# Optimization experiments

Hardware: AMD Instinct MI355X
Metric: run time of the kernel (lower is better)

Reference implementation:

```python
import jax, jax.numpy as jnp
import numpy as np

B, NPTS, T, P, C, D = 2, 32768, 32768, 512, 4, 768


def _sincos_pos_embed(centers, embed_dim):
    # centers: np [P,3]; matches get_3d_sincos_pos_embed
    c = centers - centers.mean(axis=0)
    c = c / np.linalg.norm(c, axis=1).max()
    div = np.exp(np.arange(0, embed_dim, 6) * -(np.log(10000.0) / embed_dim))  # [D/6]
    arg = c[:, None, :] * div[None, :, None]                                   # [P, D/6, 3]
    pe = np.concatenate([np.sin(arg), np.cos(arg)], axis=-1).reshape(centers.shape[0], embed_dim)
    return pe.astype(np.float32)


def setup_inputs() -> dict:
    key = jax.random.key(0)
    ks = jax.random.split(key, 12)
    rng = np.random.default_rng(0)

    # ragged patch sizes (avg 64) summing exactly to T
    sizes = rng.integers(32, 97, size=P).astype(np.int64)
    sizes = np.maximum((sizes * (T / sizes.sum())).astype(np.int64), 1)
    sizes[-1] += T - sizes.sum()
    patch_offset = jnp.asarray(np.concatenate([[0], np.cumsum(sizes)]), dtype=jnp.int32)  # [P+1]

    patch_index = jax.random.randint(ks[0], (T,), 0, NPTS, dtype=jnp.int32)
    latent = jax.random.normal(ks[1], (B, NPTS, C), dtype=jnp.float32)

    s = 0.02
    params = dict(
        w1a=jax.random.normal(ks[2], (C, D), jnp.float32) * s,
        b1a=jnp.zeros((D,), jnp.float32),
        w1b=jax.random.normal(ks[3], (D, D), jnp.float32) * s,
        b1b=jnp.zeros((D,), jnp.float32),
        w2a=jax.random.normal(ks[4], (2 * D, D), jnp.float32) * s,
        b2a=jnp.zeros((D,), jnp.float32),
        g2=jnp.ones((D,), jnp.float32),
        beta2=jnp.zeros((D,), jnp.float32),
        w2b=jax.random.normal(ks[5], (D, D), jnp.float32) * s,
        b2b=jnp.zeros((D,), jnp.float32),
    )

    centers = rng.standard_normal((P, 3))
    pos_embed = jnp.asarray(_sincos_pos_embed(centers, D))[None]  # [1, P, D]

    return dict(latent=latent, patch_index=patch_index, patch_offset=patch_offset,
                pos_embed=pos_embed, **params)


def _ln(x, eps, gamma=None, beta=None):
    mu = x.mean(axis=-1, keepdims=True)
    var = ((x - mu) ** 2).mean(axis=-1, keepdims=True)
    y = (x - mu) * jax.lax.rsqrt(var + eps)
    if gamma is not None:
        y = y * gamma + beta
    return y


def reference(latent, patch_index, patch_offset, pos_embed,
              w1a, b1a, w1b, b1b, w2a, b2a, g2, beta2, w2b, b2b):
    T_ = patch_index.shape[0]
    P_ = patch_offset.shape[0] - 1
    # segment id of each token (repeat_interleave inverse): seg[t] = patch containing t
    seg = jnp.searchsorted(patch_offset[1:], jnp.arange(T_, dtype=patch_offset.dtype), side='right')

    x = latent[:, patch_index, :]                           # [B, T, C] gather
    h = x @ w1a + b1a
    h = jax.nn.gelu(_ln(h, 1e-6), approximate=False)
    h = h @ w1b + b1b                                       # [B, T, D]

    segmax = lambda a: jax.ops.segment_max(a, seg, num_segments=P_)
    y = jax.vmap(segmax)(h)                                 # [B, P, D] ragged max-pool

    h2 = jnp.concatenate([y[:, seg, :], h], axis=-1)        # repeat_interleave + concat
    h2 = h2 @ w2a + b2a
    h2 = jax.nn.gelu(_ln(h2, 1e-5, g2, beta2), approximate=False)
    h2 = h2 @ w2b + b2b                                     # [B, T, D]
    raw_latent = h2

    out = jax.vmap(segmax)(raw_latent) + pos_embed          # [B, P, D]
    return out.astype(raw_latent.dtype), raw_latent
```

## Files before the change

### kernel.cpp

```cpp
#include <hip/hip_runtime.h>
#include <hip/hip_bf16.h>
#include <math.h>

#define B_    2
#define NPTS_ 32768
#define T_    32768
#define P_    512
#define C_    4
#define D_    768
#define M_    (B_ * T_)

typedef __bf16 bf16_t;
typedef __bf16 bf16x8 __attribute__((ext_vector_type(8)));
typedef __bf16 bf16x4 __attribute__((ext_vector_type(4)));
typedef float  f32x4  __attribute__((ext_vector_type(4)));

__device__ inline void gload16(const void* g, void* l) {
  __builtin_amdgcn_global_load_lds(
      (const __attribute__((address_space(1))) void*)g,
      (__attribute__((address_space(3))) void*)l, 16, 0, 0);
}

__device__ inline float gelu_exact(float x) {
  return 0.5f * x * (1.0f + erff(x * 0.70710678118654752f));
}

__device__ inline unsigned fmap(float x) {
  unsigned u = __float_as_uint(x);
  return (u & 0x80000000u) ? ~u : (u | 0x80000000u);
}
__device__ inline float funmap(unsigned u) {
  unsigned v = (u & 0x80000000u) ? (u & 0x7FFFFFFFu) : ~u;
  return __uint_as_float(v);
}

__global__ void seg_kernel(const int* __restrict__ off, int* __restrict__ seg) {
  int t = blockIdx.x * blockDim.x + threadIdx.x;
  if (t >= T_) return;
  int lo = 0, hi = P_;
  while (lo < hi) {
    int mid = (lo + hi) >> 1;
    if (off[mid + 1] <= t) lo = mid + 1; else hi = mid;
  }
  seg[t] = lo;
}

__global__ __launch_bounds__(256) void init_umax_kernel(uint4* __restrict__ u) {
  u[blockIdx.x * 256 + threadIdx.x] = make_uint4(0, 0, 0, 0);
}

__global__ __launch_bounds__(256) void yconv_kernel(
    const uint4* __restrict__ ymax, bf16_t* __restrict__ y) {
  int t = blockIdx.x * 256 + threadIdx.x;
  uint4 u = ymax[t];
  bf16x4 o;
  o[0] = (bf16_t)funmap(u.x); o[1] = (bf16_t)funmap(u.y);
  o[2] = (bf16_t)funmap(u.z); o[3] = (bf16_t)funmap(u.w);
  *(bf16x4*)(y + (size_t)t * 4) = o;
}

__global__ __launch_bounds__(256) void final2_kernel(
    const uint4* __restrict__ rmax, const float4* __restrict__ pe,
    float4* __restrict__ out) {
  int t = blockIdx.x * 256 + threadIdx.x;
  int row = t / 192, col = t % 192;
  uint4 u = rmax[t];
  float4 p = pe[(row & (P_ - 1)) * 192 + col];
  float4 o;
  o.x = funmap(u.x) + p.x; o.y = funmap(u.y) + p.y;
  o.z = funmap(u.z) + p.z; o.w = funmap(u.w) + p.w;
  out[t] = o;
}

__global__ __launch_bounds__(256) void wconvT_kernel(
    const float* __restrict__ src, bf16_t* __restrict__ dst, int K, int N) {
  __shared__ float tile[32][33];
  int n0 = blockIdx.x * 32, k0 = blockIdx.y * 32;
  int tx = threadIdx.x, ty = threadIdx.y;
  #pragma unroll
  for (int i = 0; i < 4; ++i)
    tile[ty + 8 * i][tx] = src[(size_t)(k0 + ty + 8 * i) * N + n0 + tx];
  __syncthreads();
  #pragma unroll
  for (int i = 0; i < 4; ++i)
    dst[(size_t)(n0 + ty + 8 * i) * K + k0 + tx] = (bf16_t)tile[tx][ty + 8 * i];
}

__global__ __launch_bounds__(256) void embed_kernel(
    const float4* __restrict__ latent4, const int* __restrict__ pidx,
    const float* __restrict__ w1a, const float* __restrict__ b1a,
    bf16_t* __restrict__ act1) {
  int wid = threadIdx.x >> 6, lane = threadIdx.x & 63;
  int m = blockIdx.x * 4 + wid;
  int b = m >> 15, t = m & (T_ - 1);
  float4 x = latent4[(size_t)b * NPTS_ + pidx[t]];
  int d8 = lane * 8, d4 = 512 + lane * 4;
  float v[12];
  {
    float4 a0 = *(const float4*)(b1a + d8);
    float4 a1 = *(const float4*)(b1a + d8 + 4);
    float4 a2 = *(const float4*)(b1a + d4);
    v[0]=a0.x; v[1]=a0.y; v[2]=a0.z; v[3]=a0.w;
    v[4]=a1.x; v[5]=a1.y; v[6]=a1.z; v[7]=a1.w;
    v[8]=a2.x; v[9]=a2.y; v[10]=a2.z; v[11]=a2.w;
  }
  float xk[4] = {x.x, x.y, x.z, x.w};
  #pragma unroll
  for (int k = 0; k < 4; ++k) {
    const float* w = w1a + k * D_;
    float4 w0 = *(const float4*)(w + d8);
    float4 w1 = *(const float4*)(w + d8 + 4);
    float4 w2 = *(const float4*)(w + d4);
    float f = xk[k];
    v[0] += f*w0.x; v[1] += f*w0.y; v[2] += f*w0.z; v[3] += f*w0.w;
    v[4] += f*w1.x; v[5] += f*w1.y; v[6] += f*w1.z; v[7] += f*w1.w;
    v[8] += f*w2.x; v[9] += f*w2.y; v[10]+= f*w2.z; v[11]+= f*w2.w;
  }
  float sum = 0.f, sq = 0.f;
  #pragma unroll
  for (int j = 0; j < 12; ++j) { sum += v[j]; sq += v[j]*v[j]; }
  #pragma unroll
  for (int o = 32; o > 0; o >>= 1) { sum += __shfl_xor(sum, o); sq += __shfl_xor(sq, o); }
  float mu = sum * (1.0f / D_);
  float rstd = rsqrtf(sq * (1.0f / D_) - mu * mu + 1e-6f);
  bf16x8 o8; bf16x4 o4;
  #pragma unroll
  for (int j = 0; j < 8; ++j) o8[j] = (bf16_t)gelu_exact((v[j] - mu) * rstd);
  #pragma unroll
  for (int j = 0; j < 4; ++j) o4[j] = (bf16_t)gelu_exact((v[8 + j] - mu) * rstd);
  size_t base = (size_t)m * D_;
  *(bf16x8*)(act1 + base + d8) = o8;
  *(bf16x4*)(act1 + base + d4) = o4;
}

__global__ __launch_bounds__(256) void ln2_kernel(
    const bf16_t* __restrict__ h2pre, const float* __restrict__ z,
    const int* __restrict__ seg, const float* __restrict__ g2,
    const float* __restrict__ beta2, bf16_t* __restrict__ act2) {
  int wid = threadIdx.x >> 6, lane = threadIdx.x & 63;
  int m = blockIdx.x * 4 + wid;
  int b = m >> 15, t = m & (T_ - 1);
  int d8 = lane * 8, d4 = 512 + lane * 4;
  size_t base = (size_t)m * D_;
  const float* zrow = z + (size_t)((b << 9) + seg[t]) * D_;
  bf16x8 i8 = *(const bf16x8*)(h2pre + base + d8);
  bf16x4 i4 = *(const bf16x4*)(h2pre + base + d4);
  float4 z0 = *(const float4*)(zrow + d8);
  float4 z1 = *(const float4*)(zrow + d8 + 4);
  float4 z2 = *(const float4*)(zrow + d4);
  float v[12];
  #pragma unroll
  for (int j = 0; j < 8; ++j) v[j] = (float)i8[j];
  #pragma unroll
  for (int j = 0; j < 4; ++j) v[8 + j] = (float)i4[j];
  v[0]+=z0.x; v[1]+=z0.y; v[2]+=z0.z; v[3]+=z0.w;
  v[4]+=z1.x; v[5]+=z1.y; v[6]+=z1.z; v[7]+=z1.w;
  v[8]+=z2.x; v[9]+=z2.y; v[10]+=z2.z; v[11]+=z2.w;
  float sum = 0.f, sq = 0.f;
  #pragma unroll
  for (int j = 0; j < 12; ++j) { sum += v[j]; sq += v[j]*v[j]; }
  #pragma unroll
  for (int o = 32; o > 0; o >>= 1) { sum += __shfl_xor(sum, o); sq += __shfl_xor(sq, o); }
  float mu = sum * (1.0f / D_);
  float rstd = rsqrtf(sq * (1.0f / D_) - mu * mu + 1e-5f);
  float4 ga = *(const float4*)(g2 + d8);
  float4 gb = *(const float4*)(g2 + d8 + 4);
  float4 gc = *(const float4*)(g2 + d4);
  float4 ba = *(const float4*)(beta2 + d8);
  float4 bb = *(const float4*)(beta2 + d8 + 4);
  float4 bc = *(const float4*)(beta2 + d4);
  float g[12] = {ga.x,ga.y,ga.z,ga.w, gb.x,gb.y,gb.z,gb.w, gc.x,gc.y,gc.z,gc.w};
  float be[12]= {ba.x,ba.y,ba.z,ba.w, bb.x,bb.y,bb.z,bb.w, bc.x,bc.y,bc.z,bc.w};
  bf16x8 o8; bf16x4 o4;
  #pragma unroll
  for (int j = 0; j < 8; ++j) o8[j] = (bf16_t)gelu_exact((v[j] - mu) * rstd * g[j] + be[j]);
  #pragma unroll
  for (int j = 0; j < 4; ++j) o4[j] = (bf16_t)gelu_exact((v[8+j] - mu) * rstd * g[8+j] + be[8+j]);
  *(bf16x8*)(act2 + base + d8) = o8;
  *(bf16x4*)(act2 + base + d4) = o4;
}

#define STAGE_A(P2, KTG)                                                     \
  { _Pragma("unroll")                                                        \
    for (int h = 0; h < 2; ++h) {                                            \
      _Pragma("unroll")                                                      \
      for (int ps = 0; ps < 2; ++ps) {                                       \
        int c = ps * 512 + wid * 64 + lane;                                  \
        int rw = c >> 3;                                                     \
        int cs = (c & 7) ^ (rw & 7);                                         \
        gload16(A + (size_t)(m0 + h * 128 + rw) * 768 + (KTG) + cs * 8,      \
                lds + (P2) * 65536 + h * 16384 + ps * 8192 + wid * 1024);    \
      } } }

#define STAGE_B(P2, KTG)                                                     \
  { _Pragma("unroll")                                                        \
    for (int h = 0; h < 2; ++h) {                                            \
      _Pragma("unroll")                                                      \
      for (int ps = 0; ps < 2; ++ps) {                                       \
        int c = ps * 512 + wid * 64 + lane;                                  \
        int rw = c >> 3;                                                     \
        int cs = (c & 7) ^ (rw & 7);                                         \
        gload16(BT + (size_t)(n0 + h * 128 + rw) * 768 + (KTG) + cs * 8,     \
                lds + (P2) * 65536 + 32768 + h * 16384 + ps * 8192 + wid * 1024); \
      } } }

template <bool HASBIAS, bool SEGMAX, typename OutT>
__global__ __launch_bounds__(512, 1) void gemm256_kernel(
    const bf16_t* __restrict__ A, const bf16_t* __restrict__ BT,
    const float* __restrict__ bias, OutT* __restrict__ C,
    const int* __restrict__ seg, unsigned* __restrict__ gmax) {
  constexpr int NT = 12;
  __shared__ __align__(16) char lds[131072];
  __shared__ int segm[256];
  int tid = threadIdx.x;
  int wid = tid >> 6, lane = tid & 63;
  int lr = lane & 15, hi = lane >> 4;
  int wm = wid >> 2, wn = wid & 3;

  int gx = gridDim.x;
  int nb = gx * gridDim.y;
  int bid = blockIdx.y * gx + blockIdx.x;
  int w = ((nb & 7) == 0) ? ((bid & 7) * (nb >> 3) + (bid >> 3)) : bid;
  int bx = w % gx, by = w / gx;
  int n0 = bx * 256, m0 = by * 256;

  if (SEGMAX) { if (tid < 256) segm[tid] = seg[(m0 + tid) & (T_ - 1)]; }

  f32x4 acc[8][4] = {};
  bf16x8 af0[4][2], af1[4][2], bf0[2][2], bf1[2][2];
  int cx = lr & 7;

  STAGE_A(0, 0); STAGE_B(0, 0);
  STAGE_A(1, 64); STAGE_B(1, 64);

  for (int j = 0; j < NT; ++j) {
    int p = j & 1;
    const char* base = lds + p * 65536;
    if (j < NT - 1) asm volatile("s_waitcnt vmcnt(8)" ::: "memory");
    else            asm volatile("s_waitcnt vmcnt(0)" ::: "memory");
    __builtin_amdgcn_s_barrier();
    #pragma unroll
    for (int i = 0; i < 4; ++i)
      #pragma unroll
      for (int s = 0; s < 2; ++s) {
        int row = i * 16 + lr;
        int ch = (s * 4 + hi) ^ cx;
        af0[i][s] = *(const bf16x8*)(base + wm * 16384 + row * 128 + ch * 16);
      }
    #pragma unroll
    for (int jb = 0; jb < 2; ++jb)
      #pragma unroll
      for (int s = 0; s < 2; ++s) {
        int nrow = wn * 64 + jb * 16 + lr;
        int ch = (s * 4 + hi) ^ cx;
        bf0[jb][s] = *(const bf16x8*)(base + 32768 + (nrow >> 7) * 16384 +
                                      (nrow & 127) * 128 + ch * 16);
      }
    __builtin_amdgcn_s_barrier();
    __builtin_amdgcn_s_setprio(1);
    #pragma unroll
    for (int i = 0; i < 4; ++i)
      #pragma unroll
      for (int jb = 0; jb < 2; ++jb)
        #pragma unroll
        for (int s = 0; s < 2; ++s)
          acc[i][jb] = __builtin_amdgcn_mfma_f32_16x16x32_bf16(af0[i][s], bf0[jb][s], acc[i][jb], 0, 0, 0);
    __builtin_amdgcn_s_setprio(0);
    __builtin_amdgcn_s_barrier();

    #pragma unroll
    for (int i = 0; i < 4; ++i)
      #pragma unroll
      for (int s = 0; s < 2; ++s) {
        int row = 64 + i * 16 + lr;
        int ch = (s * 4 + hi) ^ cx;
        af1[i][s] = *(const bf16x8*)(base + wm * 16384 + row * 128 + ch * 16);
      }
    __builtin_amdgcn_s_barrier();
    __builtin_amdgcn_s_setprio(1);
    #pragma unroll
    for (int i = 0; i < 4; ++i)
      #pragma unroll
      for (int jb = 0; jb < 2; ++jb)
        #pragma unroll
        for (int s = 0; s < 2; ++s)
          acc[4 + i][jb] = __builtin_amdgcn_mfma_f32_16x16x32_bf16(af1[i][s], bf0[jb][s], acc[4 + i][jb], 0, 0, 0);
    __builtin_amdgcn_s_setprio(0);
    __builtin_amdgcn_s_barrier();

    #pragma unroll
    for (int jb = 0; jb < 2; ++jb)
      #pragma unroll
      for (int s = 0; s < 2; ++s) {
        int nrow = wn * 64 + 32 + jb * 16 + lr;
        int ch = (s * 4 + hi) ^ cx;
        bf1[jb][s] = *(const bf16x8*)(base + 32768 + (nrow >> 7) * 16384 +
                                      (nrow & 127) * 128 + ch * 16);
      }
    if (j + 2 < NT) STAGE_A(p, (j + 2) * 64);
    __builtin_amdgcn_s_barrier();
    __builtin_amdgcn_s_setprio(1);
    #pragma unroll
    for (int i = 0; i < 4; ++i)
      #pragma unroll
      for (int jb = 0; jb < 2; ++jb)
        #pragma unroll
        for (int s = 0; s < 2; ++s)
          acc[i][2 + jb] = __builtin_amdgcn_mfma_f32_16x16x32_bf16(af0[i][s], bf1[jb][s], acc[i][2 + jb], 0, 0, 0);
    __builtin_amdgcn_s_setprio(0);
    __builtin_amdgcn_s_barrier();

    if (j + 2 < NT) STAGE_B(p, (j + 2) * 64);
    __builtin_amdgcn_s_barrier();
    __builtin_amdgcn_s_setprio(1);
    #pragma unroll
    for (int i = 0; i < 4; ++i)
      #pragma unroll
      for (int jb = 0; jb < 2; ++jb)
        #pragma unroll
        for (int s = 0; s < 2; ++s)
          acc[4 + i][2 + jb] = __builtin_amdgcn_mfma_f32_16x16x32_bf16(af1[i][s], bf1[jb][s], acc[4 + i][2 + jb], 0, 0, 0);
    __builtin_amdgcn_s_setprio(0);
  }

  unsigned* smax = reinterpret_cast<unsigned*>(lds);
  int sb = 0, zb = 0;
  if (SEGMAX) {
    __builtin_amdgcn_s_barrier();
    sb = segm[0];
    zb = (m0 >> 15) << 9;
    for (int q = tid; q < 16 * 256; q += 512) smax[q] = 0u;
    __syncthreads();
  }

  #pragma unroll
  for (int jn = 0; jn < 4; ++jn) {
    int nl = wn * 64 + jn * 16 + lr;
    int n = n0 + nl;
    float bv = HASBIAS ? bias[n] : 0.f;
    #pragma unroll
    for (int i = 0; i < 8; ++i) {
      int rb = wm * 128 + i * 16 + hi * 4;
      float vv[4];
      #pragma unroll
      for (int r = 0; r < 4; ++r) {
        vv[r] = acc[i][jn][r] + bv;
        C[(size_t)(m0 + rb + r) * 768 + n] = (OutT)vv[r];
      }
      if (SEGMAX) {
        int sA = segm[rb] - sb, sB = segm[rb + 3] - sb;
        if (sA == sB) {
          float mx = fmaxf(fmaxf(vv[0], vv[1]), fmaxf(vv[2], vv[3]));
          atomicMax(&smax[sA * 256 + nl], fmap(mx));
        } else {
          #pragma unroll
          for (int r = 0; r < 4; ++r)
            atomicMax(&smax[(segm[rb + r] - sb) * 256 + nl], fmap(vv[r]));
        }
      }
    }
  }

  if (SEGMAX) {
    __syncthreads();
    int nseg = segm[255] - sb + 1;
    for (int q = tid; q < nseg * 256; q += 512) {
      int sl = q >> 8, nl2 = q & 255;
      atomicMax(&gmax[(size_t)(zb + sb + sl) * 768 + n0 + nl2], smax[q]);
    }
  }
}

extern "C" void kernel_launch(void* const* d_in, const int* in_sizes, int n_in,
                              void* d_out, int out_size, void* d_ws, size_t ws_size,
                              hipStream_t stream) {
  const float* latent       = (const float*)d_in[0];
  const int*   patch_index  = (const int*)d_in[1];
  const int*   patch_offset = (const int*)d_in[2];
  const float* pos_embed    = (const float*)d_in[3];
  const float* w1a  = (const float*)d_in[4];
  const float* b1a  = (const float*)d_in[5];
  const float* w1b  = (const float*)d_in[6];
  const float* b1b  = (const float*)d_in[7];
  const float* w2a  = (const float*)d_in[8];
  const float* b2a  = (const float*)d_in[9];
  const float* g2   = (const float*)d_in[10];
  const float* beta2= (const float*)d_in[11];
  const float* w2b  = (const float*)d_in[12];
  const float* b2b  = (const float*)d_in[13];

  float* out_f   = (float*)d_out;
  float* raw_out = out_f + (size_t)B_ * P_ * D_;

  char* ws = (char*)d_ws;
  size_t off = 0;
  auto take = [&](size_t bytes) {
    off = (off + 255) & ~(size_t)255;
    char* p = ws + off;
    off += bytes;
    return p;
  };
  int*      seg   = (int*)     take((size_t)T_ * 4);
  bf16_t*   w1bT  = (bf16_t*)  take((size_t)D_ * D_ * 2);
  bf16_t*   w2aTT = (bf16_t*)  take((size_t)D_ * D_ * 2);
  bf16_t*   w2aBT = (bf16_t*)  take((size_t)D_ * D_ * 2);
  bf16_t*   w2bT  = (bf16_t*)  take((size_t)D_ * D_ * 2);
  bf16_t*   ybuf  = (bf16_t*)  take((size_t)B_ * P_ * D_ * 2);
  float*    zbuf  = (float*)   take((size_t)B_ * P_ * D_ * 4);
  unsigned* umax  = (unsigned*)take((size_t)2 * B_ * P_ * D_ * 4);
  unsigned* ymax  = umax;
  unsigned* rmax  = umax + (size_t)B_ * P_ * D_;
  bf16_t*   bufY  = (bf16_t*)  take((size_t)M_ * D_ * 2);
  size_t needX = (size_t)M_ * D_ * 2;
  size_t offX  = (off + 255) & ~(size_t)255;
  bf16_t* bufX;
  if (offX + needX <= ws_size) {
    bufX = (bf16_t*)take(needX);
  } else {
    bufX = (bf16_t*)raw_out;
  }

  seg_kernel<<<(T_ + 255) / 256, 256, 0, stream>>>(patch_offset, seg);
  init_umax_kernel<<<(2 * B_ * P_ * D_) / (4 * 256), 256, 0, stream>>>((uint4*)umax);
  dim3 wcb(32, 8);
  wconvT_kernel<<<dim3(D_/32, D_/32), wcb, 0, stream>>>(w1b, w1bT, D_, D_);
  wconvT_kernel<<<dim3(D_/32, D_/32), wcb, 0, stream>>>(w2a, w2aTT, D_, D_);
  wconvT_kernel<<<dim3(D_/32, D_/32), wcb, 0, stream>>>(w2a + (size_t)D_*D_, w2aBT, D_, D_);
  wconvT_kernel<<<dim3(D_/32, D_/32), wcb, 0, stream>>>(w2b, w2bT, D_, D_);

  embed_kernel<<<M_ / 4, 256, 0, stream>>>((const float4*)latent, patch_index, w1a, b1a, bufX);

  gemm256_kernel<true, true, bf16_t><<<dim3(3, M_/256), 512, 0, stream>>>(
      bufX, w1bT, b1b, bufY, seg, ymax);

  yconv_kernel<<<(B_ * P_ * D_) / (4 * 256), 256, 0, stream>>>((const uint4*)ymax, ybuf);

  gemm256_kernel<true, false, float><<<dim3(3, (B_*P_)/256), 512, 0, stream>>>(
      ybuf, w2aTT, b2a, zbuf, nullptr, nullptr);

  gemm256_kernel<false, false, bf16_t><<<dim3(3, M_/256), 512, 0, stream>>>(
      bufY, w2aBT, nullptr, bufX, nullptr, nullptr);

  ln2_kernel<<<M_ / 4, 256, 0, stream>>>(bufX, zbuf, seg, g2, beta2, bufY);

  gemm256_kernel<true, true, float><<<dim3(3, M_/256), 512, 0, stream>>>(
      bufY, w2bT, b2b, raw_out, seg, rmax);

  final2_kernel<<<(B_ * P_ * D_) / (4 * 256), 256, 0, stream>>>(
      (const uint4*)rmax, (const float4*)pos_embed, (float4*)out_f);
}
```

Before: 456.9 us.

## Prefetch next K-tile fragments early and cut barriers in GEMM main loop

Restructures the double-buffered GEMM main loop so the next iteration's A0/B0 LDS fragments are read before the final MFMA quadrant, overlapping LDS reads with compute across iterations. Barriers per iteration drop, and the vmcnt waits are rebalanced so B staging is issued after the prefetch. This trades more register pressure and subtler hazard reasoning for less synchronization stall.

```diff
diff --git a/kernel.cpp b/kernel.cpp
--- a/kernel.cpp
+++ b/kernel.cpp
@@ -204,6 +204,27 @@
                 lds + (P2) * 65536 + 32768 + h * 16384 + ps * 8192 + wid * 1024); \
       } } }
 
+#define READ_AF0(BASE)                                                       \
+  { _Pragma("unroll")                                                        \
+    for (int i = 0; i < 4; ++i) {                                            \
+      _Pragma("unroll")                                                      \
+      for (int s = 0; s < 2; ++s) {                                          \
+        int row = i * 16 + lr;                                               \
+        int ch = (s * 4 + hi) ^ cx;                                          \
+        af0[i][s] = *(const bf16x8*)((BASE) + wm * 16384 + row * 128 + ch * 16); \
+      } } }
+
+#define READ_BF0(BASE)                                                       \
+  { _Pragma("unroll")                                                        \
+    for (int jb = 0; jb < 2; ++jb) {                                         \
+      _Pragma("unroll")                                                      \
+      for (int s = 0; s < 2; ++s) {                                          \
+        int nrow = wn * 64 + jb * 16 + lr;                                   \
+        int ch = (s * 4 + hi) ^ cx;                                          \
+        bf0[jb][s] = *(const bf16x8*)((BASE) + 32768 + (nrow >> 7) * 16384 + \
+                                      (nrow & 127) * 128 + ch * 16);         \
+      } } }
+
 template <bool HASBIAS, bool SEGMAX, typename OutT>
 __global__ __launch_bounds__(512, 1) void gemm256_kernel(
     const bf16_t* __restrict__ A, const bf16_t* __restrict__ BT,
@@ -232,31 +253,22 @@
 
   STAGE_A(0, 0); STAGE_B(0, 0);
   STAGE_A(1, 64); STAGE_B(1, 64);
+  asm volatile("s_waitcnt vmcnt(8)" ::: "memory");
+  __builtin_amdgcn_s_barrier();
+  READ_AF0(lds); READ_BF0(lds);
 
   for (int j = 0; j < NT; ++j) {
-    int p = j & 1;
-    const char* base = lds + p * 65536;
-    if (j < NT - 1) asm volatile("s_waitcnt vmcnt(8)" ::: "memory");
-    else            asm volatile("s_waitcnt vmcnt(0)" ::: "memory");
-    __builtin_amdgcn_s_barrier();
+    const char* base  = lds + (j & 1) * 65536;
+    const char* baseN = lds + ((j & 1) ^ 1) * 65536;
+
     #pragma unroll
     for (int i = 0; i < 4; ++i)
       #pragma unroll
       for (int s = 0; s < 2; ++s) {
-        int row = i * 16 + lr;
+        int row = 64 + i * 16 + lr;
         int ch = (s * 4 + hi) ^ cx;
-        af0[i][s] = *(const bf16x8*)(base + wm * 16384 + row * 128 + ch * 16);
+        af1[i][s] = *(const bf16x8*)(base + wm * 16384 + row * 128 + ch * 16);
       }
-    #pragma unroll
-    for (int jb = 0; jb < 2; ++jb)
-      #pragma unroll
-      for (int s = 0; s < 2; ++s) {
-        int nrow = wn * 64 + jb * 16 + lr;
-        int ch = (s * 4 + hi) ^ cx;
-        bf0[jb][s] = *(const bf16x8*)(base + 32768 + (nrow >> 7) * 16384 +
-                                      (nrow & 127) * 128 + ch * 16);
-      }
-    __builtin_amdgcn_s_barrier();
     __builtin_amdgcn_s_setprio(1);
     #pragma unroll
     for (int i = 0; i < 4; ++i)
@@ -269,14 +281,14 @@
     __builtin_amdgcn_s_barrier();
 
     #pragma unroll
-    for (int i = 0; i < 4; ++i)
+    for (int jb = 0; jb < 2; ++jb)
       #pragma unroll
       for (int s = 0; s < 2; ++s) {
-        int row = 64 + i * 16 + lr;
+        int nrow = wn * 64 + 32 + jb * 16 + lr;
         int ch = (s * 4 + hi) ^ cx;
-        af1[i][s] = *(const bf16x8*)(base + wm * 16384 + row * 128 + ch * 16);
+        bf1[jb][s] = *(const bf16x8*)(base + 32768 + (nrow >> 7) * 16384 +
+                                      (nrow & 127) * 128 + ch * 16);
       }
-    __builtin_amdgcn_s_barrier();
     __builtin_amdgcn_s_setprio(1);
     #pragma unroll
     for (int i = 0; i < 4; ++i)
@@ -288,17 +300,7 @@
     __builtin_amdgcn_s_setprio(0);
     __builtin_amdgcn_s_barrier();
 
-    #pragma unroll
-    for (int jb = 0; jb < 2; ++jb)
-      #pragma unroll
-      for (int s = 0; s < 2; ++s) {
-        int nrow = wn * 64 + 32 + jb * 16 + lr;
-        int ch = (s * 4 + hi) ^ cx;
-        bf1[jb][s] = *(const bf16x8*)(base + 32768 + (nrow >> 7) * 16384 +
-                                      (nrow & 127) * 128 + ch * 16);
-      }
-    if (j + 2 < NT) STAGE_A(p, (j + 2) * 64);
-    __builtin_amdgcn_s_barrier();
+    if (j + 2 < NT) STAGE_A(j & 1, (j + 2) * 64);
     __builtin_amdgcn_s_setprio(1);
     #pragma unroll
     for (int i = 0; i < 4; ++i)
@@ -308,10 +310,14 @@
         for (int s = 0; s < 2; ++s)
           acc[i][2 + jb] = __builtin_amdgcn_mfma_f32_16x16x32_bf16(af0[i][s], bf1[jb][s], acc[i][2 + jb], 0, 0, 0);
     __builtin_amdgcn_s_setprio(0);
-    __builtin_amdgcn_s_barrier();
-
-    if (j + 2 < NT) STAGE_B(p, (j + 2) * 64);
-    __builtin_amdgcn_s_barrier();
+
+    if (j + 1 < NT) {
+      if (j + 2 < NT) asm volatile("s_waitcnt vmcnt(4)" ::: "memory");
+      else            asm volatile("s_waitcnt vmcnt(0)" ::: "memory");
+      __builtin_amdgcn_s_barrier();
+      READ_AF0(baseN); READ_BF0(baseN);
+      if (j + 2 < NT) STAGE_B(j & 1, (j + 2) * 64);
+    }
     __builtin_amdgcn_s_setprio(1);
     #pragma unroll
     for (int i = 0; i < 4; ++i)
@@ -321,12 +327,12 @@
         for (int s = 0; s < 2; ++s)
           acc[4 + i][2 + jb] = __builtin_amdgcn_mfma_f32_16x16x32_bf16(af1[i][s], bf1[jb][s], acc[4 + i][2 + jb], 0, 0, 0);
     __builtin_amdgcn_s_setprio(0);
+    __builtin_amdgcn_s_barrier();
   }
 
   unsigned* smax = reinterpret_cast<unsigned*>(lds);
   int sb = 0, zb = 0;
   if (SEGMAX) {
-    __builtin_amdgcn_s_barrier();
     sb = segm[0];
     zb = (m0 >> 15) << 9;
     for (int q = tid; q < 16 * 256; q += 512) smax[q] = 0u;
```

New measurement: 451.1 us. About the same (-1.3%).

## Fuse setup kernels into one prep launch and skip atomics for interior segments

Applied to the files above, without the earlier changes.

Six small setup launches (segment search, max-buffer zeroing, four weight transposes) are merged into one prep kernel that picks its role from the block index. The segmented-max flush in the GEMM epilogue now uses plain stores for segments wholly inside a 256-row tile and keeps atomicMax only for segments that cross the tile's edges. This removes launch overhead and some global atomic traffic. The plain-store path depends on each interior segment being written by exactly one tile per column block, and the buffer still has to be zeroed first for the boundary atomics.

```diff
diff --git a/kernel.cpp b/kernel.cpp
--- a/kernel.cpp
+++ b/kernel.cpp
@@ -34,19 +34,41 @@
   return __uint_as_float(v);
 }
 
-__global__ void seg_kernel(const int* __restrict__ off, int* __restrict__ seg) {
-  int t = blockIdx.x * blockDim.x + threadIdx.x;
-  if (t >= T_) return;
-  int lo = 0, hi = P_;
-  while (lo < hi) {
-    int mid = (lo + hi) >> 1;
-    if (off[mid + 1] <= t) lo = mid + 1; else hi = mid;
-  }
-  seg[t] = lo;
-}
-
-__global__ __launch_bounds__(256) void init_umax_kernel(uint4* __restrict__ u) {
-  u[blockIdx.x * 256 + threadIdx.x] = make_uint4(0, 0, 0, 0);
+__global__ __launch_bounds__(256) void prep_kernel(
+    const int* __restrict__ off, int* __restrict__ seg, uint4* __restrict__ umax,
+    const float* __restrict__ w1b, const float* __restrict__ w2a,
+    const float* __restrict__ w2b,
+    bf16_t* __restrict__ w1bT, bf16_t* __restrict__ w2aTT,
+    bf16_t* __restrict__ w2aBT, bf16_t* __restrict__ w2bT) {
+  __shared__ float tile[32][33];
+  int bid = blockIdx.x, tid = threadIdx.x;
+  if (bid < 2304) {
+    const float* src; bf16_t* dst;
+    int which = bid / 576, r = bid - which * 576;
+    if (which == 0)      { src = w1b;             dst = w1bT;  }
+    else if (which == 1) { src = w2a;             dst = w2aTT; }
+    else if (which == 2) { src = w2a + D_ * D_;   dst = w2aBT; }
+    else                 { src = w2b;             dst = w2bT;  }
+    int n0 = (r % 24) * 32, k0 = (r / 24) * 32;
+    int tx = tid & 31, ty = tid >> 5;
+    #pragma unroll
+    for (int i = 0; i < 4; ++i)
+      tile[ty + 8 * i][tx] = src[(size_t)(k0 + ty + 8 * i) * D_ + n0 + tx];
+    __syncthreads();
+    #pragma unroll
+    for (int i = 0; i < 4; ++i)
+      dst[(size_t)(n0 + ty + 8 * i) * D_ + k0 + tx] = (bf16_t)tile[tx][ty + 8 * i];
+  } else if (bid < 2432) {
+    int t = (bid - 2304) * 256 + tid;
+    int lo = 0, hi = P_;
+    while (lo < hi) {
+      int mid = (lo + hi) >> 1;
+      if (off[mid + 1] <= t) lo = mid + 1; else hi = mid;
+    }
+    seg[t] = lo;
+  } else {
+    umax[(size_t)(bid - 2432) * 256 + tid] = make_uint4(0, 0, 0, 0);
+  }
 }
 
 __global__ __launch_bounds__(256) void yconv_kernel(
@@ -70,20 +92,6 @@
   o.x = funmap(u.x) + p.x; o.y = funmap(u.y) + p.y;
   o.z = funmap(u.z) + p.z; o.w = funmap(u.w) + p.w;
   out[t] = o;
-}
-
-__global__ __launch_bounds__(256) void wconvT_kernel(
-    const float* __restrict__ src, bf16_t* __restrict__ dst, int K, int N) {
-  __shared__ float tile[32][33];
-  int n0 = blockIdx.x * 32, k0 = blockIdx.y * 32;
-  int tx = threadIdx.x, ty = threadIdx.y;
-  #pragma unroll
-  for (int i = 0; i < 4; ++i)
-    tile[ty + 8 * i][tx] = src[(size_t)(k0 + ty + 8 * i) * N + n0 + tx];
-  __syncthreads();
-  #pragma unroll
-  for (int i = 0; i < 4; ++i)
-    dst[(size_t)(n0 + ty + 8 * i) * K + k0 + tx] = (bf16_t)tile[tx][ty + 8 * i];
 }
 
 __global__ __launch_bounds__(256) void embed_kernel(
@@ -364,9 +372,16 @@
   if (SEGMAX) {
     __syncthreads();
     int nseg = segm[255] - sb + 1;
+    int mlo = m0 & (T_ - 1);
+    bool strad_lo = (mlo != 0) && (seg[(mlo - 1)] == sb);
+    bool strad_hi = (mlo + 256 < T_) && (seg[(mlo + 256)] == segm[255]);
     for (int q = tid; q < nseg * 256; q += 512) {
       int sl = q >> 8, nl2 = q & 255;
-      atomicMax(&gmax[(size_t)(zb + sb + sl) * 768 + n0 + nl2], smax[q]);
+      unsigned val = smax[q];
+      unsigned* dst = &gmax[(size_t)(zb + sb + sl) * 768 + n0 + nl2];
+      bool bdry = (sl == 0 && strad_lo) || (sl == nseg - 1 && strad_hi);
+      if (bdry) atomicMax(dst, val);
+      else      *dst = val;
     }
   }
 }
@@ -420,13 +435,8 @@
     bufX = (bf16_t*)raw_out;
   }
 
-  seg_kernel<<<(T_ + 255) / 256, 256, 0, stream>>>(patch_offset, seg);
-  init_umax_kernel<<<(2 * B_ * P_ * D_) / (4 * 256), 256, 0, stream>>>((uint4*)umax);
-  dim3 wcb(32, 8);
-  wconvT_kernel<<<dim3(D_/32, D_/32), wcb, 0, stream>>>(w1b, w1bT, D_, D_);
-  wconvT_kernel<<<dim3(D_/32, D_/32), wcb, 0, stream>>>(w2a, w2aTT, D_, D_);
-  wconvT_kernel<<<dim3(D_/32, D_/32), wcb, 0, stream>>>(w2a + (size_t)D_*D_, w2aBT, D_, D_);
-  wconvT_kernel<<<dim3(D_/32, D_/32), wcb, 0, stream>>>(w2b, w2bT, D_, D_);
+  prep_kernel<<<3968, 256, 0, stream>>>(patch_offset, seg, (uint4*)umax,
+                                        w1b, w2a, w2b, w1bT, w2aTT, w2aBT, w2bT);
 
   embed_kernel<<<M_ / 4, 256, 0, stream>>>((const float4*)latent, patch_index, w1a, b1a, bufX);
 
```

Result: no change. 452.3 us (-1.0%).
